# Optimization experiments

Measured on AMD Instinct MI355X. Metric: run time of the kernel, lower is better.

## Reference

```python
import jax, jax.numpy as jnp
import numpy as np

BN_EPS = 1e-5
LRELU_SLOPE = 0.2


def _knn(x, k):
    # x: (B, C, N). Returns idx (B, N, k) of k nearest neighbors (incl. self).
    inner = -2.0 * jnp.einsum('bcn,bcm->bnm', x, x)          # (B, N, N)
    xx = jnp.sum(x * x, axis=1)                               # (B, N)
    dist = -xx[:, :, None] - inner - xx[:, None, :]           # negative sq. distance
    _, idx = jax.lax.top_k(dist, k)                           # (B, N, k)
    return idx


def setup_inputs() -> dict:
    key = jax.random.key(0)
    k1, k2 = jax.random.split(key)
    B, C, N, O, K = 8, 64, 4096, 64, 16
    x = jax.random.normal(k1, (B, C, N), dtype=jnp.float32)
    W = jax.random.normal(k2, (O, 2 * C), dtype=jnp.float32) * (1.0 / np.sqrt(2 * C))
    gamma = jnp.ones((O,), dtype=jnp.float32)
    beta = jnp.zeros((O,), dtype=jnp.float32)
    return {"x": x, "W": W, "gamma": gamma, "beta": beta, "k": K}


def reference(x, W, gamma, beta, k):
    # x: (B, C, N); W: (O, 2C) 1x1 conv weight; BN in training mode (batch stats).
    idx = _knn(x, k)                                          # (B, N, k) int32
    x_t = jnp.transpose(x, (0, 2, 1))                         # (B, N, C)
    neighbor = jax.vmap(lambda xt, i: xt[i])(x_t, idx)        # (B, N, k, C)
    center = x_t[:, :, None, :]                               # (B, N, 1, C)
    feat = jnp.concatenate(
        (neighbor - center, jnp.broadcast_to(center, neighbor.shape)), axis=-1
    )                                                         # (B, N, k, 2C)
    y = jnp.einsum('bnkc,oc->bonk', feat, W)                  # (B, O, N, k)
    # BatchNorm2d (training mode): stats over (B, N, k) per channel
    mean = jnp.mean(y, axis=(0, 2, 3), keepdims=True)
    var = jnp.var(y, axis=(0, 2, 3), keepdims=True)
    y = (y - mean) * jax.lax.rsqrt(var + BN_EPS)
    y = y * gamma[None, :, None, None] + beta[None, :, None, None]
    y = jnp.where(y >= 0, y, LRELU_SLOPE * y)                 # LeakyReLU(0.2)
    return jnp.max(y, axis=-1)                                # (B, O, N)
```

## Files before the change

kernel.cpp:

```cpp
#include <hip/hip_runtime.h>

#define NPTS 4096
#define NCH  64
#define NB   8
#define KNN  16
#define NSPLIT 4

typedef _Float16 h8 __attribute__((ext_vector_type(8)));
typedef float    f4 __attribute__((ext_vector_type(4)));
typedef unsigned long long ull;

__global__ __launch_bounds__(256) void k_prep(const float* __restrict__ x,
                                              double* __restrict__ xm,
                                              _Float16* __restrict__ xhT,
                                              _Float16* __restrict__ xlT) {
    __shared__ float tile[64 * 65];
    const int tid = threadIdx.x;
    const int blk = blockIdx.x;
    const int b = blk >> 6, n0 = (blk & 63) << 6;
    const float* xb = x + (size_t)b * NCH * NPTS;
    for (int i = tid; i < 4096; i += 256) {
        int c = i >> 6, nn = i & 63;
        tile[c * 65 + nn] = xb[(size_t)c * NPTS + n0 + nn];
    }
    __syncthreads();
    if (tid < 64) {
        double a = 0.0;
        #pragma unroll
        for (int c = 0; c < 64; ++c) {
            double v = (double)tile[c * 65 + tid];
            a = fma(v, v, a);
        }
        xm[((size_t)b << 12) + n0 + tid] = 4096.0 - a;
    }
    for (int i = tid; i < 4096; i += 256) {
        int n = i >> 6, c = i & 63;
        float v = tile[c * 65 + n];
        _Float16 h = (_Float16)v;
        _Float16 l = (_Float16)(v - (float)h);
        size_t o = (((size_t)b << 12) + n0 + n) * 64 + c;
        xhT[o] = h;
        xlT[o] = l;
    }
}

__global__ __launch_bounds__(256) void k_knn(const float* __restrict__ x,
                                             const double* __restrict__ xm,
                                             const _Float16* __restrict__ xhT,
                                             const _Float16* __restrict__ xlT,
                                             double* __restrict__ part) {
    __shared__ int okflag;
    const int tid = threadIdx.x, lane = tid & 63, w = tid >> 6;
    const int g = lane >> 4, j = lane & 15;
    const int b = blockIdx.y, q0 = blockIdx.x * 64;
    const int split = blockIdx.z;
    const int t0 = split * 16;
    const size_t bbase = (size_t)b << 12;
    const _Float16* Hb = xhT + bbase * 64;
    const _Float16* Lb = xlT + bbase * 64;
    const double*  xmb = xm + bbase;

    const int qcol = q0 + 16 * w + j;
    h8 Bh[2], Bl[2];
    #pragma unroll
    for (int kk = 0; kk < 2; ++kk) {
        size_t o = (size_t)qcol * 64 + kk * 32 + 8 * g;
        Bh[kk] = *(const h8*)(Hb + o);
        Bl[kk] = *(const h8*)(Lb + o);
    }

    if (tid == 0) okflag = 1;
    __syncthreads();

    {
        const int rsh = q0 + 16 * w + ((j + 1) & 15);
        f4 acc = {0.f, 0.f, 0.f, 0.f};
        #pragma unroll
        for (int kk = 0; kk < 2; ++kk) {
            size_t o = (size_t)rsh * 64 + kk * 32 + 8 * g;
            h8 Ah = *(const h8*)(Hb + o);
            h8 Al = *(const h8*)(Lb + o);
            acc = __builtin_amdgcn_mfma_f32_16x16x32_f16(Ah, Bh[kk], acc, 0, 0, 0);
            acc = __builtin_amdgcn_mfma_f32_16x16x32_f16(Ah, Bl[kk], acc, 0, 0, 0);
            acc = __builtin_amdgcn_mfma_f32_16x16x32_f16(Al, Bh[kk], acc, 0, 0, 0);
        }
        bool bad = false;
        #pragma unroll
        for (int rr = 0; rr < 2; ++rr) {
            const int r = rr ? 3 : 0;
            const int urow = q0 + 16 * w + ((4 * g + r + 1) & 15);
            double tgt = 0.0;
            #pragma unroll 4
            for (int c = 0; c < 64; ++c) {
                double av = (double)(float)Hb[(size_t)urow * 64 + c]
                          + (double)(float)Lb[(size_t)urow * 64 + c];
                double bv = (double)(float)Hb[(size_t)qcol * 64 + c]
                          + (double)(float)Lb[(size_t)qcol * 64 + c];
                tgt = fma(av, bv, tgt);
            }
            double got = (double)acc[r];
            if (fabs(got - tgt) > 1e-3 * (1.0 + fabs(tgt))) bad = true;
        }
        if (__any(bad ? 1 : 0)) okflag = 0;
    }
    __syncthreads();
    const bool mfma_ok = (okflag != 0);

    double s[16];
    #pragma unroll
    for (int i = 0; i < 16; ++i) s[i] = 0.0;

    if (mfma_ok) {
        for (int t = t0; t < t0 + 16; ++t) {
            const int m0 = t * 64;
            #pragma unroll
            for (int mt = 0; mt < 4; ++mt) {
                const int arow = m0 + 16 * mt + j;
                f4 acc = {0.f, 0.f, 0.f, 0.f};
                #pragma unroll
                for (int kk = 0; kk < 2; ++kk) {
                    size_t o = (size_t)arow * 64 + kk * 32 + 8 * g;
                    h8 Ah = *(const h8*)(Hb + o);
                    h8 Al = *(const h8*)(Lb + o);
                    acc = __builtin_amdgcn_mfma_f32_16x16x32_f16(Ah, Bh[kk], acc, 0, 0, 0);
                    acc = __builtin_amdgcn_mfma_f32_16x16x32_f16(Ah, Bl[kk], acc, 0, 0, 0);
                    acc = __builtin_amdgcn_mfma_f32_16x16x32_f16(Al, Bh[kk], acc, 0, 0, 0);
                }
                const int mbase = m0 + 16 * mt + 4 * g;
                #pragma unroll
                for (int r = 0; r < 4; ++r) {
                    const int m = mbase + r;
                    double pv = fma(2.0, (double)acc[r], xmb[m]);
                    ull bits = (((ull)__double_as_longlong(pv)) & 0xFFFFFFFFFFFFF000ULL)
                             | (ull)(4095 - m);
                    double v = __longlong_as_double((long long)bits);
                    #pragma unroll
                    for (int i = 0; i < 15; ++i) s[i] = fmin(s[i + 1], fmax(v, s[i]));
                    s[15] = fmax(v, s[15]);
                }
            }
        }
    } else {
        const float* xb = x + (size_t)b * NCH * NPTS;
        for (int t = t0; t < t0 + 16; ++t) {
            const int m0 = t * 64;
            #pragma unroll
            for (int mt = 0; mt < 4; ++mt) {
                #pragma unroll
                for (int r = 0; r < 4; ++r) {
                    const int m = m0 + 16 * mt + 4 * g + r;
                    double dot = 0.0;
                    for (int c = 0; c < 64; ++c)
                        dot = fma((double)xb[(size_t)c * NPTS + m],
                                  (double)xb[(size_t)c * NPTS + qcol], dot);
                    double pv = fma(2.0, dot, xmb[m]);
                    ull bits = (((ull)__double_as_longlong(pv)) & 0xFFFFFFFFFFFFF000ULL)
                             | (ull)(4095 - m);
                    double v = __longlong_as_double((long long)bits);
                    #pragma unroll
                    for (int i = 0; i < 15; ++i) s[i] = fmin(s[i + 1], fmax(v, s[i]));
                    s[15] = fmax(v, s[15]);
                }
            }
        }
    }

    #pragma unroll
    for (int i = 0; i < 16; ++i) {
        double v = __shfl(s[i], (lane + 32) & 63, 64);
        if (g < 2) {
            #pragma unroll
            for (int k2 = 0; k2 < 15; ++k2) s[k2] = fmin(s[k2 + 1], fmax(v, s[k2]));
            s[15] = fmax(v, s[15]);
        }
    }
    #pragma unroll
    for (int i = 0; i < 16; ++i) {
        double v = __shfl(s[i], (lane + 16) & 63, 64);
        if (g == 0) {
            #pragma unroll
            for (int k2 = 0; k2 < 15; ++k2) s[k2] = fmin(s[k2 + 1], fmax(v, s[k2]));
            s[15] = fmax(v, s[15]);
        }
    }
    if (g == 0) {
        const size_t qi = bbase + q0 + 16 * w + j;
        #pragma unroll
        for (int i = 0; i < 16; ++i)
            part[(size_t)(split * 16 + i) * (NB * NPTS) + qi] = s[i];
    }
}

__global__ __launch_bounds__(256) void k_kmerge(const double* __restrict__ part,
                                                int* __restrict__ idx_out) {
    const int qi = blockIdx.x * 256 + threadIdx.x;
    double tb[16];
    #pragma unroll
    for (int i = 0; i < 16; ++i) tb[i] = 0.0;
    for (int sp = 0; sp < NSPLIT; ++sp) {
        #pragma unroll
        for (int i = 0; i < 16; ++i) {
            double v = part[(size_t)(sp * 16 + i) * (NB * NPTS) + qi];
            #pragma unroll
            for (int k2 = 0; k2 < 15; ++k2) tb[k2] = fmin(tb[k2 + 1], fmax(v, tb[k2]));
            tb[15] = fmax(v, tb[15]);
        }
    }
    int* op = idx_out + (size_t)qi * KNN;
    #pragma unroll
    for (int i = 0; i < 16; ++i) {
        int code = (int)((ull)__double_as_longlong(tb[i]) & 0xFFFULL);
        op[i] = 4095 - code;
    }
}

__global__ __launch_bounds__(256) void k_pq(const float* __restrict__ x,
                                            const float* __restrict__ W,
                                            float* __restrict__ P,
                                            float* __restrict__ Q) {
    __shared__ __align__(16) float sX[4096];
    __shared__ __align__(16) float sWt[8192];
    const int tid = threadIdx.x;
    const int g0  = blockIdx.x * 64;
    const int b   = g0 >> 12;
    const int n0  = g0 & 4095;
    const float* xb = x + (size_t)b * NCH * NPTS;

    for (int i = tid; i < 8192; i += 256) {
        int c = i >> 7, oc = i & 127;
        float wv;
        if (oc < 64) wv = W[oc * 128 + c];
        else { int o = oc - 64; wv = W[o * 128 + 64 + c] - W[o * 128 + c]; }
        sWt[c * 128 + oc] = wv;
    }
    for (int i = tid; i < 4096; i += 256) {
        int c = i >> 6, m = i & 63;
        sX[i] = xb[(size_t)c * NPTS + n0 + m];
    }
    __syncthreads();

    const int ty = tid >> 4, tx = tid & 15;
    float aP[4][4], aQ[4][4];
    #pragma unroll
    for (int i = 0; i < 4; ++i)
        #pragma unroll
        for (int jj = 0; jj < 4; ++jj) { aP[i][jj] = 0.f; aQ[i][jj] = 0.f; }

    const float4* a4 = (const float4*)sX + ty;
    const float4* p4 = (const float4*)sWt + tx;
    const float4* q4 = (const float4*)sWt + 16 + tx;
    #pragma unroll 8
    for (int kk = 0; kk < 64; ++kk) {
        float4 a  = a4[kk * 16];
        float4 wp = p4[kk * 32];
        float4 wq = q4[kk * 32];
        aP[0][0] = fmaf(a.x, wp.x, aP[0][0]); aP[0][1] = fmaf(a.x, wp.y, aP[0][1]);
        aP[0][2] = fmaf(a.x, wp.z, aP[0][2]); aP[0][3] = fmaf(a.x, wp.w, aP[0][3]);
        aP[1][0] = fmaf(a.y, wp.x, aP[1][0]); aP[1][1] = fmaf(a.y, wp.y, aP[1][1]);
        aP[1][2] = fmaf(a.y, wp.z, aP[1][2]); aP[1][3] = fmaf(a.y, wp.w, aP[1][3]);
        aP[2][0] = fmaf(a.z, wp.x, aP[2][0]); aP[2][1] = fmaf(a.z, wp.y, aP[2][1]);
        aP[2][2] = fmaf(a.z, wp.z, aP[2][2]); aP[2][3] = fmaf(a.z, wp.w, aP[2][3]);
        aP[3][0] = fmaf(a.w, wp.x, aP[3][0]); aP[3][1] = fmaf(a.w, wp.y, aP[3][1]);
        aP[3][2] = fmaf(a.w, wp.z, aP[3][2]); aP[3][3] = fmaf(a.w, wp.w, aP[3][3]);
        aQ[0][0] = fmaf(a.x, wq.x, aQ[0][0]); aQ[0][1] = fmaf(a.x, wq.y, aQ[0][1]);
        aQ[0][2] = fmaf(a.x, wq.z, aQ[0][2]); aQ[0][3] = fmaf(a.x, wq.w, aQ[0][3]);
        aQ[1][0] = fmaf(a.y, wq.x, aQ[1][0]); aQ[1][1] = fmaf(a.y, wq.y, aQ[1][1]);
        aQ[1][2] = fmaf(a.y, wq.z, aQ[1][2]); aQ[1][3] = fmaf(a.y, wq.w, aQ[1][3]);
        aQ[2][0] = fmaf(a.z, wq.x, aQ[2][0]); aQ[2][1] = fmaf(a.z, wq.y, aQ[2][1]);
        aQ[2][2] = fmaf(a.z, wq.z, aQ[2][2]); aQ[2][3] = fmaf(a.z, wq.w, aQ[2][3]);
        aQ[3][0] = fmaf(a.w, wq.x, aQ[3][0]); aQ[3][1] = fmaf(a.w, wq.y, aQ[3][1]);
        aQ[3][2] = fmaf(a.w, wq.z, aQ[3][2]); aQ[3][3] = fmaf(a.w, wq.w, aQ[3][3]);
    }
    #pragma unroll
    for (int i = 0; i < 4; ++i) {
        size_t row = (size_t)(g0 + ty * 4 + i) * 64;
        float4 vp; vp.x = aP[i][0]; vp.y = aP[i][1]; vp.z = aP[i][2]; vp.w = aP[i][3];
        float4 vq; vq.x = aQ[i][0]; vq.y = aQ[i][1]; vq.z = aQ[i][2]; vq.w = aQ[i][3];
        ((float4*)(P + row))[tx] = vp;
        ((float4*)(Q + row))[tx] = vq;
    }
}

__global__ __launch_bounds__(256) void k_stats(const float* __restrict__ P,
                                               const float* __restrict__ Q,
                                               const int* __restrict__ idx,
                                               float* __restrict__ Mx,
                                               float* __restrict__ Mn,
                                               float* __restrict__ gsum,
                                               float* __restrict__ gsum2) {
    const int tid = threadIdx.x;
    const int o = tid & 63, ng = tid >> 6;
    const int b = blockIdx.y;
    const int n0 = blockIdx.x * 16;
    const float* Pb = P + (((size_t)b << 12) * 64);
    float ssum = 0.f, ssq = 0.f;
    for (int jj = 0; jj < 4; ++jj) {
        int n = n0 + ng * 4 + jj;
        size_t base = ((size_t)b << 12) + n;
        float qv = Q[base * 64 + o];
        const int* ip = idx + base * 16;
        float vmax = -3.4e38f, vmin = 3.4e38f;
        #pragma unroll
        for (int k = 0; k < 16; ++k) {
            int m = ip[k];
            float v = Pb[(size_t)m * 64 + o] + qv;
            vmax = fmaxf(vmax, v);
            vmin = fminf(vmin, v);
            ssum += v;
            ssq  = fmaf(v, v, ssq);
        }
        Mx[base * 64 + o] = vmax;
        Mn[base * 64 + o] = vmin;
    }
    __shared__ float red[8][64];
    red[ng][o] = ssum;
    red[ng + 4][o] = ssq;
    __syncthreads();
    if (tid < 64) {
        float ss  = red[0][o] + red[1][o] + red[2][o] + red[3][o];
        float ss2 = red[4][o] + red[5][o] + red[6][o] + red[7][o];
        atomicAdd(&gsum[o], ss);
        atomicAdd(&gsum2[o], ss2);
    }
}

__global__ __launch_bounds__(256) void k_final(const float* __restrict__ Mx,
                                               const float* __restrict__ Mn,
                                               const float* __restrict__ gsum,
                                               const float* __restrict__ gsum2,
                                               const float* __restrict__ gamma,
                                               const float* __restrict__ beta,
                                               float* __restrict__ out) {
    __shared__ float tX[64 * 65], tN[64 * 65];
    const int tid = threadIdx.x;
    const int b = blockIdx.y;
    const int n0 = blockIdx.x * 64;
    size_t base = ((size_t)b << 12) + n0;
    for (int i = tid; i < 4096; i += 256) {
        int nl = i >> 6, o = i & 63;
        tX[nl * 65 + o] = Mx[(base + nl) * 64 + o];
        tN[nl * 65 + o] = Mn[(base + nl) * 64 + o];
    }
    __syncthreads();
    const int lane = tid & 63, wv = tid >> 6;
    const float inv = 1.0f / 524288.0f;
    for (int oo = 0; oo < 16; ++oo) {
        int o = wv * 16 + oo;
        float mean = gsum[o] * inv;
        float var  = gsum2[o] * inv - mean * mean;
        float scv  = gamma[o] * rsqrtf(var + 1e-5f);
        float bsv  = beta[o] - mean * scv;
        float M = (scv >= 0.f) ? tX[lane * 65 + o] : tN[lane * 65 + o];
        float v = fmaf(scv, M, bsv);
        out[((size_t)b * 64 + o) * 4096 + n0 + lane] = (v >= 0.f) ? v : 0.2f * v;
    }
}

extern "C" void kernel_launch(void* const* d_in, const int* in_sizes, int n_in,
                              void* d_out, int out_size, void* d_ws, size_t ws_size,
                              hipStream_t stream) {
    const float* x     = (const float*)d_in[0];
    const float* W     = (const float*)d_in[1];
    const float* gamma = (const float*)d_in[2];
    const float* beta  = (const float*)d_in[3];
    float* out = (float*)d_out;

    char* ws = (char*)d_ws;
    double*    xm    = (double*)(ws);
    float*     gsum  = (float*)(ws + 262144);
    float*     gsum2 = (float*)(ws + 262400);
    int*       idx   = (int*)  (ws + 393216);
    _Float16*  xhT   = (_Float16*)(ws + 2490368);
    _Float16*  xlT   = (_Float16*)(ws + 6684672);
    float*     P     = (float*)(ws + 10878976);
    float*     Q     = (float*)(ws + 19267584);
    double*    part  = (double*)(ws + 10878976);
    float*     Mx    = (float*)(ws + 2490368);
    float*     Mn    = (float*)(ws + 27656192);

    hipMemsetAsync(gsum, 0, 512, stream);
    k_prep  <<<dim3(512),        256, 0, stream>>>(x, xm, xhT, xlT);
    k_knn   <<<dim3(64, 8, 4),   256, 0, stream>>>(x, xm, xhT, xlT, part);
    k_kmerge<<<dim3(128),        256, 0, stream>>>(part, idx);
    k_pq    <<<dim3(512),        256, 0, stream>>>(x, W, P, Q);
    k_stats <<<dim3(256, 8),     256, 0, stream>>>(P, Q, idx, Mx, Mn, gsum, gsum2);
    k_final <<<dim3(64, 8),      256, 0, stream>>>(Mx, Mn, gsum, gsum2, gamma, beta, out);
}
```

Measured before the change: 529.9 us.

## Replace insertion top-k with bitonic sort-merge and drop the split-merge kernel

The per-candidate insertion update of the 16-element top-k list is replaced by a block scheme. Each tile of 16 candidates is sorted with a bitonic network, combined elementwise with the running list, and cleaned up with a bitonic merge. This cuts the fmin/fmax work per candidate. The KNN kernel no longer splits the candidate range four ways across blockIdx.z: it scans all points and writes indices directly, so the partial buffer and the k_kmerge launch go away. The trade-off is four times fewer blocks, which lowers occupancy, and each thread does a longer serial scan.

```diff
diff --git a/kernel.cpp b/kernel.cpp
--- a/kernel.cpp
+++ b/kernel.cpp
@@ -4,11 +4,45 @@
 #define NCH  64
 #define NB   8
 #define KNN  16
-#define NSPLIT 4
 
 typedef _Float16 h8 __attribute__((ext_vector_type(8)));
 typedef float    f4 __attribute__((ext_vector_type(4)));
 typedef unsigned long long ull;
+
+__device__ __forceinline__ void sort16_desc(double* d) {
+    #pragma unroll
+    for (int k2 = 2; k2 <= 16; k2 <<= 1) {
+        #pragma unroll
+        for (int j2 = k2 >> 1; j2 > 0; j2 >>= 1) {
+            #pragma unroll
+            for (int i = 0; i < 16; ++i) {
+                int l = i ^ j2;
+                if (l > i) {
+                    double lo = fmin(d[i], d[l]);
+                    double hi = fmax(d[i], d[l]);
+                    bool up = ((i & k2) == 0);
+                    d[i] = up ? hi : lo;
+                    d[l] = up ? lo : hi;
+                }
+            }
+        }
+    }
+}
+
+__device__ __forceinline__ void bmerge16_asc(double* s) {
+    #pragma unroll
+    for (int j2 = 8; j2 > 0; j2 >>= 1) {
+        #pragma unroll
+        for (int i = 0; i < 16; ++i) {
+            int l = i ^ j2;
+            if (l > i) {
+                double lo = fmin(s[i], s[l]);
+                double hi = fmax(s[i], s[l]);
+                s[i] = lo; s[l] = hi;
+            }
+        }
+    }
+}
 
 __global__ __launch_bounds__(256) void k_prep(const float* __restrict__ x,
                                               double* __restrict__ xm,
@@ -48,17 +82,16 @@
                                              const double* __restrict__ xm,
                                              const _Float16* __restrict__ xhT,
                                              const _Float16* __restrict__ xlT,
-                                             double* __restrict__ part) {
+                                             int* __restrict__ idx_out) {
     __shared__ int okflag;
     const int tid = threadIdx.x, lane = tid & 63, w = tid >> 6;
     const int g = lane >> 4, j = lane & 15;
     const int b = blockIdx.y, q0 = blockIdx.x * 64;
-    const int split = blockIdx.z;
-    const int t0 = split * 16;
     const size_t bbase = (size_t)b << 12;
     const _Float16* Hb = xhT + bbase * 64;
     const _Float16* Lb = xlT + bbase * 64;
     const double*  xmb = xm + bbase;
+    const float*   xb  = x + (size_t)b * NCH * NPTS;
 
     const int qcol = q0 + 16 * w + j;
     h8 Bh[2], Bl[2];
@@ -110,9 +143,10 @@
     #pragma unroll
     for (int i = 0; i < 16; ++i) s[i] = 0.0;
 
-    if (mfma_ok) {
-        for (int t = t0; t < t0 + 16; ++t) {
-            const int m0 = t * 64;
+    for (int t = 0; t < 64; ++t) {
+        const int m0 = t * 64;
+        double d[16];
+        if (mfma_ok) {
             #pragma unroll
             for (int mt = 0; mt < 4; ++mt) {
                 const int arow = m0 + 16 * mt + j;
@@ -133,17 +167,10 @@
                     double pv = fma(2.0, (double)acc[r], xmb[m]);
                     ull bits = (((ull)__double_as_longlong(pv)) & 0xFFFFFFFFFFFFF000ULL)
                              | (ull)(4095 - m);
-                    double v = __longlong_as_double((long long)bits);
-                    #pragma unroll
-                    for (int i = 0; i < 15; ++i) s[i] = fmin(s[i + 1], fmax(v, s[i]));
-                    s[15] = fmax(v, s[15]);
+                    d[mt * 4 + r] = __longlong_as_double((long long)bits);
                 }
             }
-        }
-    } else {
-        const float* xb = x + (size_t)b * NCH * NPTS;
-        for (int t = t0; t < t0 + 16; ++t) {
-            const int m0 = t * 64;
+        } else {
             #pragma unroll
             for (int mt = 0; mt < 4; ++mt) {
                 #pragma unroll
@@ -156,61 +183,39 @@
                     double pv = fma(2.0, dot, xmb[m]);
                     ull bits = (((ull)__double_as_longlong(pv)) & 0xFFFFFFFFFFFFF000ULL)
                              | (ull)(4095 - m);
-                    double v = __longlong_as_double((long long)bits);
-                    #pragma unroll
-                    for (int i = 0; i < 15; ++i) s[i] = fmin(s[i + 1], fmax(v, s[i]));
-                    s[15] = fmax(v, s[15]);
+                    d[mt * 4 + r] = __longlong_as_double((long long)bits);
                 }
             }
         }
-    }
-
-    #pragma unroll
-    for (int i = 0; i < 16; ++i) {
-        double v = __shfl(s[i], (lane + 32) & 63, 64);
+        sort16_desc(d);
+        #pragma unroll
+        for (int i = 0; i < 16; ++i) s[i] = fmax(s[i], d[i]);
+        bmerge16_asc(s);
+    }
+
+    {
+        double d2[16];
+        #pragma unroll
+        for (int i = 0; i < 16; ++i)
+            d2[i] = __shfl(s[15 - i], (lane + 32) & 63, 64);
         if (g < 2) {
             #pragma unroll
-            for (int k2 = 0; k2 < 15; ++k2) s[k2] = fmin(s[k2 + 1], fmax(v, s[k2]));
-            s[15] = fmax(v, s[15]);
-        }
-    }
-    #pragma unroll
-    for (int i = 0; i < 16; ++i) {
-        double v = __shfl(s[i], (lane + 16) & 63, 64);
+            for (int i = 0; i < 16; ++i) s[i] = fmax(s[i], d2[i]);
+            bmerge16_asc(s);
+        }
+        #pragma unroll
+        for (int i = 0; i < 16; ++i)
+            d2[i] = __shfl(s[15 - i], (lane + 16) & 63, 64);
         if (g == 0) {
             #pragma unroll
-            for (int k2 = 0; k2 < 15; ++k2) s[k2] = fmin(s[k2 + 1], fmax(v, s[k2]));
-            s[15] = fmax(v, s[15]);
-        }
-    }
-    if (g == 0) {
-        const size_t qi = bbase + q0 + 16 * w + j;
-        #pragma unroll
-        for (int i = 0; i < 16; ++i)
-            part[(size_t)(split * 16 + i) * (NB * NPTS) + qi] = s[i];
-    }
-}
-
-__global__ __launch_bounds__(256) void k_kmerge(const double* __restrict__ part,
-                                                int* __restrict__ idx_out) {
-    const int qi = blockIdx.x * 256 + threadIdx.x;
-    double tb[16];
-    #pragma unroll
-    for (int i = 0; i < 16; ++i) tb[i] = 0.0;
-    for (int sp = 0; sp < NSPLIT; ++sp) {
-        #pragma unroll
-        for (int i = 0; i < 16; ++i) {
-            double v = part[(size_t)(sp * 16 + i) * (NB * NPTS) + qi];
-            #pragma unroll
-            for (int k2 = 0; k2 < 15; ++k2) tb[k2] = fmin(tb[k2 + 1], fmax(v, tb[k2]));
-            tb[15] = fmax(v, tb[15]);
-        }
-    }
-    int* op = idx_out + (size_t)qi * KNN;
-    #pragma unroll
-    for (int i = 0; i < 16; ++i) {
-        int code = (int)((ull)__double_as_longlong(tb[i]) & 0xFFFULL);
-        op[i] = 4095 - code;
+            for (int i = 0; i < 16; ++i) s[i] = fmax(s[i], d2[i]);
+            int* op = idx_out + (bbase + (size_t)qcol) * KNN;
+            #pragma unroll
+            for (int i = 0; i < 16; ++i) {
+                int code = (int)((ull)__double_as_longlong(s[i]) & 0xFFFULL);
+                op[i] = 4095 - code;
+            }
+        }
     }
 }
 
@@ -374,15 +379,13 @@
     _Float16*  xlT   = (_Float16*)(ws + 6684672);
     float*     P     = (float*)(ws + 10878976);
     float*     Q     = (float*)(ws + 19267584);
-    double*    part  = (double*)(ws + 10878976);
     float*     Mx    = (float*)(ws + 2490368);
     float*     Mn    = (float*)(ws + 27656192);
 
     hipMemsetAsync(gsum, 0, 512, stream);
-    k_prep  <<<dim3(512),        256, 0, stream>>>(x, xm, xhT, xlT);
-    k_knn   <<<dim3(64, 8, 4),   256, 0, stream>>>(x, xm, xhT, xlT, part);
-    k_kmerge<<<dim3(128),        256, 0, stream>>>(part, idx);
-    k_pq    <<<dim3(512),        256, 0, stream>>>(x, W, P, Q);
-    k_stats <<<dim3(256, 8),     256, 0, stream>>>(P, Q, idx, Mx, Mn, gsum, gsum2);
-    k_final <<<dim3(64, 8),      256, 0, stream>>>(Mx, Mn, gsum, gsum2, gamma, beta, out);
-}
+    k_prep  <<<dim3(512),      256, 0, stream>>>(x, xm, xhT, xlT);
+    k_knn   <<<dim3(64, 8),    256, 0, stream>>>(x, xm, xhT, xlT, idx);
+    k_pq    <<<dim3(512),      256, 0, stream>>>(x, W, P, Q);
+    k_stats <<<dim3(256, 8),   256, 0, stream>>>(P, Q, idx, Mx, Mn, gsum, gsum2);
+    k_final <<<dim3(64, 8),    256, 0, stream>>>(Mx, Mn, gsum, gsum2, gamma, beta, out);
+}
```

New measurement: 451.0 us. 14.9% less time.
